# Kernel optimization log

Measured on AMD Instinct MI355X. Metric: run time of the kernel, lower is better.

Reference implementation:

```python
import jax, jax.numpy as jnp
import numpy as np

B, DIM, DIMH, DIMC = 1024, 32, 1024, 512
SQRT_HALF_PI = float(np.sqrt(np.pi / 2.0))
SQRT2 = float(np.sqrt(2.0))


def _gsp(x):
    """gaussian_softplus activation from ConditionalICNN."""
    return (SQRT_HALF_PI * x * jax.scipy.special.erf(x / SQRT2)
            + jnp.exp(-0.5 * x * x) + SQRT_HALF_PI * x) / (2.0 * SQRT_HALF_PI)


def setup_inputs() -> dict:
    key = jax.random.key(0)
    _i = [0]
    def nrm(shape, s=0.05):
        _i[0] += 1
        return jax.random.normal(jax.random.fold_in(key, _i[0]), shape, dtype=jnp.float32) * s
    inp = {
        "x": nrm((B, DIM), 1.0),
        "c": nrm((B, DIMC), 1.0),
        # w0 init: log(exp(1)-1) as in DeepConvexFlow
        "w0": jnp.full((1,), float(np.log(np.e - 1.0)), dtype=jnp.float32),
        "w1": jnp.zeros((1,), dtype=jnp.float32),
        "Wz0_w": nrm((DIMH, DIM)), "Wz0_b": nrm((DIMH,)),
        "Wc0_w": nrm((DIMH, DIMC)), "Wc0_b": nrm((DIMH,)),
        "an0_b": nrm((DIMH,)), "an0_logs": nrm((DIMH,), 0.01),
        "Wz1_w": nrm((DIMH, DIMH)), "Wz1_b": nrm((DIMH,)),
        "Wx1_w": nrm((DIMH, DIM)), "Wx1_b": nrm((DIMH,)),
        "Wc1_w": nrm((DIMH, DIMC)), "Wc1_b": nrm((DIMH,)),
        "an1_b": nrm((DIMH,)), "an1_logs": nrm((DIMH,), 0.01),
        "Wz2_w": nrm((DIMH, DIMH)), "Wz2_b": nrm((DIMH,)),
        "Wx2_w": nrm((DIMH, DIM)), "Wx2_b": nrm((DIMH,)),
        "Wc2_w": nrm((DIMH, DIMC)), "Wc2_b": nrm((DIMH,)),
        "an2_b": nrm((DIMH,)), "an2_logs": nrm((DIMH,), 0.01),
        "Wzout_w": nrm((1, DIMH)), "Wxout_w": nrm((1, DIM)), "Wcout_w": nrm((1, DIMC)),
    }
    return inp


def reference(x, c, w0, w1,
              Wz0_w, Wz0_b, Wc0_w, Wc0_b, an0_b, an0_logs,
              Wz1_w, Wz1_b, Wx1_w, Wx1_b, Wc1_w, Wc1_b, an1_b, an1_logs,
              Wz2_w, Wz2_b, Wx2_w, Wx2_b, Wc2_w, Wc2_b, an2_b, an2_logs,
              Wzout_w, Wxout_w, Wcout_w):
    """ConditionalDeepConvexFlow.forward_transform with exact logdet.
    Returns (f = grad_x F(x), logdet = logabsdet of per-sample Hessian)."""

    def pot(x1, c1):  # scalar convex potential F for one sample
        h = Wz0_w @ x1 + Wz0_b + Wc0_w @ c1 + Wc0_b
        z = _gsp((h + an0_b) * jnp.exp(an0_logs))  # ActNormNoLogdet + act
        for (Wz_w, Wz_b, Wx_w, Wx_b, Wc_w, Wc_b, an_b, an_logs) in (
                (Wz1_w, Wz1_b, Wx1_w, Wx1_b, Wc1_w, Wc1_b, an1_b, an1_logs),
                (Wz2_w, Wz2_b, Wx2_w, Wx2_b, Wc2_w, Wc2_b, an2_b, an2_logs)):
            # PosLinear: softplus(W) with gain 1/in_features
            h = (jax.nn.softplus(Wz_w) @ z) / DIMH + Wz_b \
                + Wx_w @ x1 + Wx_b + Wc_w @ c1 + Wc_b
            z = _gsp((h + an_b) * jnp.exp(an_logs))
        icnn = (jax.nn.softplus(Wzout_w) @ z)[0] / DIMH \
               + (Wxout_w @ x1)[0] + (Wcout_w @ c1)[0]
        return jax.nn.softplus(w1)[0] * icnn \
               + jax.nn.softplus(w0)[0] * 0.5 * jnp.sum(x1 * x1)

    f = jax.vmap(jax.grad(pot))(x, c)          # [B, DIM]
    H = jax.vmap(jax.hessian(pot))(x, c)       # [B, DIM, DIM]
    logdet = jnp.linalg.slogdet(H)[1]          # [B]
    return f, logdet
```

## Files before the change

### kernel.cpp

```cpp
#include <hip/hip_runtime.h>

constexpr int NB   = 1024;
constexpr int NDIM = 32;
constexpr int NH   = 1024;
constexpr int NC   = 512;
constexpr int NS   = 8;
constexpr int KSF  = 8;

constexpr float INV_SQRT2PI = 0.3989422804014327f;
constexpr float SQRT_HALF   = 0.70710678118654752f;
constexpr float SQRT_HPI    = 1.2533141373155003f;

typedef __attribute__((ext_vector_type(8))) short short8;
typedef __attribute__((ext_vector_type(4))) short short4v;
typedef __attribute__((ext_vector_type(4))) float float4v;

__device__ __forceinline__ float sp_f(float x) {
  return (x > 20.f) ? x : log1pf(expf(x));
}

__device__ __forceinline__ short f2bf(float f) {
  union { float f; unsigned u; } x; x.f = f;
  const unsigned r = x.u + 0x7fffu + ((x.u >> 16) & 1u);
  return (short)(r >> 16);
}

__device__ __forceinline__ float bf2f(short s) {
  union { unsigned u; float f; } c;
  c.u = ((unsigned)(unsigned short)s) << 16;
  return c.f;
}

__device__ __forceinline__ void async_ld16(const void* g, void* l) {
  __builtin_amdgcn_global_load_lds(
      (const __attribute__((address_space(1))) void*)g,
      (__attribute__((address_space(3))) void*)l, 16, 0, 0);
}

__global__ __launch_bounds__(256) void k_prep(
    const float* __restrict__ Wz1, const float* __restrict__ Wz2,
    const float* __restrict__ Wzout, const float* __restrict__ Wz0,
    const float* __restrict__ Wx1, const float* __restrict__ Wx2,
    const float* __restrict__ Wc0, const float* __restrict__ Wc1,
    const float* __restrict__ Wc2, const float* __restrict__ Cc,
    short* __restrict__ S1b, short* __restrict__ S1Tb,
    short* __restrict__ S2b, short* __restrict__ S2Tb,
    short* __restrict__ Wc0b, short* __restrict__ Wc1b, short* __restrict__ Wc2b,
    short* __restrict__ Ccb, short* __restrict__ W0Tb,
    short* __restrict__ Wx1Tb, short* __restrict__ Wx2Tb,
    float* __restrict__ so)
{
  const int idx = blockIdx.x * 256 + threadIdx.x;
  const int i = idx >> 10, p = idx & 1023;
  const float v1 = sp_f(Wz1[idx]);
  const short b1 = f2bf(v1);
  S1b[idx] = b1; S1Tb[p * NH + i] = b1;
  const float v2 = sp_f(Wz2[idx]);
  const short b2 = f2bf(v2);
  S2b[idx] = b2; S2Tb[p * NH + i] = b2;
  if (idx < NH) so[idx] = sp_f(Wzout[idx]);
  if (idx < NH * NC) {
    Wc0b[idx] = f2bf(Wc0[idx]);
    Wc1b[idx] = f2bf(Wc1[idx]);
    Wc2b[idx] = f2bf(Wc2[idx]);
  }
  if (idx < NB * NC) Ccb[idx] = f2bf(Cc[idx]);
  if (idx < NDIM * NH) {
    const int j = idx >> 10, pp = idx & 1023;
    W0Tb[idx]  = f2bf(Wz0[pp * NDIM + j]);
    Wx1Tb[idx] = f2bf(Wx1[pp * NDIM + j]);
    Wx2Tb[idx] = f2bf(Wx2[pp * NDIM + j]);
  }
}

__global__ __launch_bounds__(256) void k_gemmx(
    const float* __restrict__ A,
    const float* __restrict__ B0, const float* __restrict__ B1,
    const float* __restrict__ B2,
    float* __restrict__ C0, float* __restrict__ C1, float* __restrict__ C2,
    int ldc,
    const float* __restrict__ bz0, const float* __restrict__ bc0,
    const float* __restrict__ anb0, const float* __restrict__ anl0,
    short* __restrict__ Z0b, float* __restrict__ G0, float* __restrict__ U0)
{
  const float* Bt = (blockIdx.z == 0) ? B0 : (blockIdx.z == 1) ? B1 : B2;
  float* C        = (blockIdx.z == 0) ? C0 : (blockIdx.z == 1) ? C1 : C2;
  __shared__ float As[16][68];
  __shared__ float Bs[16][68];
  const int tid  = threadIdx.y * 16 + threadIdx.x;
  const int arow = tid >> 2;
  const int acol = (tid & 3) << 2;
  const int m0 = blockIdx.y << 6;
  const int n0 = blockIdx.x << 6;

  float acc[4][4];
#pragma unroll
  for (int i = 0; i < 4; ++i)
#pragma unroll
    for (int j = 0; j < 4; ++j) acc[i][j] = 0.f;

  const int R = m0 + arow;
  for (int k0 = 0; k0 < NDIM; k0 += 16) {
    const float4 av = *reinterpret_cast<const float4*>(&A[(size_t)R * NDIM + k0 + acol]);
    As[acol + 0][arow] = av.x; As[acol + 1][arow] = av.y;
    As[acol + 2][arow] = av.z; As[acol + 3][arow] = av.w;
    const float4 bv = *reinterpret_cast<const float4*>(&Bt[(size_t)(n0 + arow) * NDIM + k0 + acol]);
    Bs[acol + 0][arow] = bv.x; Bs[acol + 1][arow] = bv.y;
    Bs[acol + 2][arow] = bv.z; Bs[acol + 3][arow] = bv.w;
    __syncthreads();
#pragma unroll
    for (int kk = 0; kk < 16; ++kk) {
      const float4 a  = *reinterpret_cast<const float4*>(&As[kk][threadIdx.y << 2]);
      const float4 bb = *reinterpret_cast<const float4*>(&Bs[kk][threadIdx.x << 2]);
      const float am[4] = {a.x, a.y, a.z, a.w};
      const float bn[4] = {bb.x, bb.y, bb.z, bb.w};
#pragma unroll
      for (int i2 = 0; i2 < 4; ++i2)
#pragma unroll
        for (int j2 = 0; j2 < 4; ++j2)
          acc[i2][j2] = fmaf(am[i2], bn[j2], acc[i2][j2]);
    }
    __syncthreads();
  }
#pragma unroll
  for (int i2 = 0; i2 < 4; ++i2) {
    const int row = m0 + (threadIdx.y << 2) + i2;
    const int col = n0 + (threadIdx.x << 2);
    float* cp = &C[(size_t)row * ldc + col];
    const float4 cur = *reinterpret_cast<const float4*>(cp);
    float o[4];
    o[0] = acc[i2][0] + cur.x; o[1] = acc[i2][1] + cur.y;
    o[2] = acc[i2][2] + cur.z; o[3] = acc[i2][3] + cur.w;
    if (blockIdx.z == 0) {
      short4v zb;
      float4 g4, u4;
      float gg[4], uu[4];
#pragma unroll
      for (int e = 0; e < 4; ++e) {
        const int cc = col + e;
        const float bias = bz0[cc] + bc0[cc] + anb0[cc];
        const float el = expf(anl0[cc]);
        const float a = (o[e] + bias) * el;
        const float pdf = expf(-0.5f * a * a);
        const float er = erff(a * SQRT_HALF);
        zb[e] = f2bf((SQRT_HPI * a * er + pdf + SQRT_HPI * a) * INV_SQRT2PI);
        gg[e] = 0.5f * (1.f + er) * el;
        uu[e] = pdf * INV_SQRT2PI * el * el;
      }
      const size_t oi = (size_t)row * NH + col;
      *(short4v*)&Z0b[oi] = zb;
      g4.x = gg[0]; g4.y = gg[1]; g4.z = gg[2]; g4.w = gg[3];
      u4.x = uu[0]; u4.y = uu[1]; u4.z = uu[2]; u4.w = uu[3];
      *(float4*)&G0[oi] = g4;
      *(float4*)&U0[oi] = u4;
    } else {
      float4 ov;
      ov.x = o[0]; ov.y = o[1]; ov.z = o[2]; ov.w = o[3];
      *reinterpret_cast<float4*>(cp) = ov;
    }
  }
}

__global__ __launch_bounds__(256) void k_m128(
    const short* __restrict__ A, const short* __restrict__ Bt,
    float* __restrict__ C, float scale, int K, int ldc)
{
  __shared__ short As[128 * 32];
  __shared__ short Bs[128 * 32];
  const int tid  = threadIdx.x;
  const int wave = tid >> 6, lane = tid & 63;
  const int m0 = blockIdx.x << 7, n0 = blockIdx.y << 7;
  const int wm = (wave >> 1) << 6, wn = (wave & 1) << 6;
  const int qd = lane >> 4, md = lane & 15;
  const int sr = lane >> 2;
  const int sc = (lane & 3) << 3;

  float4v acc[4][4];
#pragma unroll
  for (int i = 0; i < 4; ++i)
#pragma unroll
    for (int j = 0; j < 4; ++j) acc[i][j] = (float4v)(0.f);

  for (int k0 = 0; k0 < K; k0 += 32) {
#pragma unroll
    for (int i = 0; i < 2; ++i) {
      const int ch  = wave * 2 + i;
      const int row = ch * 16 + sr;
      async_ld16(&A [(size_t)(m0 + row) * K + k0 + sc], &As[ch * 512]);
      async_ld16(&Bt[(size_t)(n0 + row) * K + k0 + sc], &Bs[ch * 512]);
    }
    __syncthreads();
    short8 af[4], bfr[4];
#pragma unroll
    for (int t = 0; t < 4; ++t) {
      af[t]  = *(const short8*)&As[(wm + t * 16 + md) * 32 + qd * 8];
      bfr[t] = *(const short8*)&Bs[(wn + t * 16 + md) * 32 + qd * 8];
    }
#pragma unroll
    for (int i = 0; i < 4; ++i)
#pragma unroll
      for (int j = 0; j < 4; ++j)
        acc[i][j] = __builtin_amdgcn_mfma_f32_16x16x32_bf16(bfr[j], af[i], acc[i][j], 0, 0, 0);
    __syncthreads();
  }

#pragma unroll
  for (int i = 0; i < 4; ++i) {
    const int rowg = m0 + wm + i * 16 + md;
#pragma unroll
    for (int j = 0; j < 4; ++j) {
      const int colb = n0 + wn + j * 16 + (qd << 2);
      float4 o;
      o.x = acc[i][j][0] * scale; o.y = acc[i][j][1] * scale;
      o.z = acc[i][j][2] * scale; o.w = acc[i][j][3] * scale;
      *reinterpret_cast<float4*>(&C[(size_t)rowg * ldc + colb]) = o;
    }
  }
}

template<int EPI>
__global__ __launch_bounds__(256) void k_mgemm(
    const short* __restrict__ A, const short* __restrict__ Bt,
    short* __restrict__ o1, short* __restrict__ o2,
    const float* __restrict__ gvec, const float* __restrict__ dvec,
    const short* __restrict__ wepiT,
    float scale, int K, int b0)
{
  __shared__ short As[128 * 32];
  const int tid  = threadIdx.x;
  const int wave = tid >> 6, lane = tid & 63;
  const int m0 = blockIdx.x << 7, n0 = blockIdx.y << 6;
  const int wm = (wave >> 1) << 6, wn = (wave & 1) << 5;
  const int qd = lane >> 4, md = lane & 15;
  const int sr = lane >> 2;
  const int sc = (lane & 3) << 3;

  float4v acc[4][2];
#pragma unroll
  for (int i = 0; i < 4; ++i)
#pragma unroll
    for (int j = 0; j < 2; ++j) acc[i][j] = (float4v)(0.f);

  for (int k0 = 0; k0 < K; k0 += 32) {
#pragma unroll
    for (int i = 0; i < 2; ++i) {
      const int ch = wave * 2 + i;
      async_ld16(&A[(size_t)(m0 + ch * 16 + sr) * K + k0 + sc], &As[ch * 512]);
    }
    short8 bfr[2];
#pragma unroll
    for (int t = 0; t < 2; ++t)
      bfr[t] = *(const short8*)&Bt[(size_t)(n0 + wn + t * 16 + md) * K + k0 + qd * 8];
    __syncthreads();
    short8 af[4];
#pragma unroll
    for (int t = 0; t < 4; ++t)
      af[t] = *(const short8*)&As[(wm + t * 16 + md) * 32 + qd * 8];
#pragma unroll
    for (int i = 0; i < 4; ++i)
#pragma unroll
      for (int j = 0; j < 2; ++j)
        acc[i][j] = __builtin_amdgcn_mfma_f32_16x16x32_bf16(bfr[j], af[i], acc[i][j], 0, 0, 0);
    __syncthreads();
  }

  const int bbase = b0 + ((m0 + wm) >> 5);
  const size_t bNH0 = (size_t)bbase * NH, bNH1 = bNH0 + NH;
  float4 dqA[2], dqB[2], ggA[2], ggB[2];
#pragma unroll
  for (int j = 0; j < 2; ++j) {
    const int colb = n0 + wn + j * 16 + (qd << 2);
    dqA[j] = *(const float4*)&dvec[bNH0 + colb];
    dqB[j] = *(const float4*)&dvec[bNH1 + colb];
    if constexpr (EPI == 2) {
      ggA[j] = *(const float4*)&gvec[bNH0 + colb];
      ggB[j] = *(const float4*)&gvec[bNH1 + colb];
    }
  }
#pragma unroll
  for (int i = 0; i < 4; ++i) {
    const int rowg = m0 + wm + i * 16 + md;
    const int j2 = rowg & 31;
#pragma unroll
    for (int j = 0; j < 2; ++j) {
      const int colb = n0 + wn + j * 16 + (qd << 2);
      const short4v wq = *(const short4v*)&wepiT[(size_t)j2 * NH + colb];
      const float4 dq = (i < 2) ? dqA[j] : dqB[j];
      const float dqv[4] = {dq.x, dq.y, dq.z, dq.w};
      float v[4];
      short4v o1v;
#pragma unroll
      for (int r = 0; r < 4; ++r) {
        v[r] = acc[i][j][r] * scale + bf2f(wq[r]);
        o1v[r] = f2bf(v[r] * dqv[r]);
      }
      *(short4v*)&o1[(size_t)rowg * NH + colb] = o1v;
      if constexpr (EPI == 2) {
        const float4 gg = (i < 2) ? ggA[j] : ggB[j];
        const float ggv[4] = {gg.x, gg.y, gg.z, gg.w};
        short4v o2v;
#pragma unroll
        for (int r = 0; r < 4; ++r) o2v[r] = f2bf(v[r] * ggv[r]);
        *(short4v*)&o2[(size_t)rowg * NH + colb] = o2v;
      }
    }
  }
}

__global__ __launch_bounds__(256) void k_mgemm64s(
    const short* __restrict__ A, const short* __restrict__ Bt,
    float* __restrict__ Cpart)
{
  __shared__ short As[64 * 32];
  __shared__ short Bs[64 * 32];
  const int tid  = threadIdx.x;
  const int wave = tid >> 6, lane = tid & 63;
  const int m0 = blockIdx.x << 6, n0 = blockIdx.y << 6;
  const int kb = blockIdx.z << 9;
  const int wm = (wave >> 1) << 5, wn = (wave & 1) << 5;
  const int qd = lane >> 4, md = lane & 15;
  const int sr = lane >> 2;
  const int sc = (lane & 3) << 3;

  float4v acc[2][2];
#pragma unroll
  for (int i = 0; i < 2; ++i)
#pragma unroll
    for (int j = 0; j < 2; ++j) acc[i][j] = (float4v)(0.f);

  for (int k0 = kb; k0 < kb + 512; k0 += 32) {
    const int row = wave * 16 + sr;
    async_ld16(&A [(size_t)(m0 + row) * NH + k0 + sc], &As[wave * 512]);
    async_ld16(&Bt[(size_t)(n0 + row) * NH + k0 + sc], &Bs[wave * 512]);
    __syncthreads();
    short8 af[2], bfr[2];
#pragma unroll
    for (int t = 0; t < 2; ++t) {
      af[t]  = *(const short8*)&As[(wm + t * 16 + md) * 32 + qd * 8];
      bfr[t] = *(const short8*)&Bs[(wn + t * 16 + md) * 32 + qd * 8];
    }
#pragma unroll
    for (int i = 0; i < 2; ++i)
#pragma unroll
      for (int j = 0; j < 2; ++j)
        acc[i][j] = __builtin_amdgcn_mfma_f32_16x16x32_bf16(bfr[j], af[i], acc[i][j], 0, 0, 0);
    __syncthreads();
  }

  float* out = Cpart + (size_t)blockIdx.z * NB * NH;
#pragma unroll
  for (int i = 0; i < 2; ++i) {
    const int rowg = m0 + wm + i * 16 + md;
#pragma unroll
    for (int j = 0; j < 2; ++j) {
      const int colb = n0 + wn + j * 16 + (qd << 2);
      float4 o;
      o.x = acc[i][j][0]; o.y = acc[i][j][1];
      o.z = acc[i][j][2]; o.w = acc[i][j][3];
      *reinterpret_cast<float4*>(&out[(size_t)rowg * NH + colb]) = o;
    }
  }
}

template<int FEPI>
__global__ __launch_bounds__(256) void k_mgemm64f(
    const short* __restrict__ A, const short* __restrict__ Bt,
    const float* __restrict__ auxA, const float* __restrict__ auxB,
    short* __restrict__ ob, float* __restrict__ of1,
    float scale)
{
  __shared__ short As[64 * 32];
  __shared__ short Bs[64 * 32];
  const int tid  = threadIdx.x;
  const int wave = tid >> 6, lane = tid & 63;
  const int m0 = blockIdx.x << 6, n0 = blockIdx.y << 6;
  const int wm = (wave >> 1) << 5, wn = (wave & 1) << 5;
  const int qd = lane >> 4, md = lane & 15;
  const int sr = lane >> 2;
  const int sc = (lane & 3) << 3;

  float4v acc[2][2];
#pragma unroll
  for (int i = 0; i < 2; ++i)
#pragma unroll
    for (int j = 0; j < 2; ++j) acc[i][j] = (float4v)(0.f);

  for (int k0 = 0; k0 < NH; k0 += 32) {
    const int row = wave * 16 + sr;
    async_ld16(&A [(size_t)(m0 + row) * NH + k0 + sc], &As[wave * 512]);
    async_ld16(&Bt[(size_t)(n0 + row) * NH + k0 + sc], &Bs[wave * 512]);
    __syncthreads();
    short8 af[2], bfr[2];
#pragma unroll
    for (int t = 0; t < 2; ++t) {
      af[t]  = *(const short8*)&As[(wm + t * 16 + md) * 32 + qd * 8];
      bfr[t] = *(const short8*)&Bs[(wn + t * 16 + md) * 32 + qd * 8];
    }
#pragma unroll
    for (int i = 0; i < 2; ++i)
#pragma unroll
      for (int j = 0; j < 2; ++j)
        acc[i][j] = __builtin_amdgcn_mfma_f32_16x16x32_bf16(bfr[j], af[i], acc[i][j], 0, 0, 0);
    __syncthreads();
  }

#pragma unroll
  for (int i = 0; i < 2; ++i) {
    const int rowg = m0 + wm + i * 16 + md;
#pragma unroll
    for (int j = 0; j < 2; ++j) {
      const int colb = n0 + wn + j * 16 + (qd << 2);
      const size_t oi = (size_t)rowg * NH + colb;
      const float4 g4 = *(const float4*)&auxA[oi];
      const float4 u4 = *(const float4*)&auxB[oi];
      const float gv[4] = {g4.x, g4.y, g4.z, g4.w};
      const float uv[4] = {u4.x, u4.y, u4.z, u4.w};
      short4v eb;
      float sd[4];
#pragma unroll
      for (int r = 0; r < 4; ++r) {
        const float t = acc[i][j][r] * scale;
        eb[r] = f2bf(t * gv[r]);
        if constexpr (FEPI == 3) sd[r] = sqrtf(fmaxf(t * uv[r], 0.f));
        else                     sd[r] = t * uv[r];
      }
      *(short4v*)&ob[oi] = eb;
      float4 s4; s4.x = sd[0]; s4.y = sd[1]; s4.z = sd[2]; s4.w = sd[3];
      *(float4*)&of1[oi] = s4;
    }
  }
}

__global__ __launch_bounds__(256) void k_act(
    const float* __restrict__ HP2, const float* __restrict__ HPC_l,
    const float* __restrict__ bA, const float* __restrict__ bB,
    const float* __restrict__ bC,
    const float* __restrict__ anb, const float* __restrict__ anl,
    short* __restrict__ Zbf, float* __restrict__ G, float* __restrict__ U,
    float scale)
{
  const int idx = blockIdx.x * 256 + threadIdx.x;
  const int i = idx & 1023;
  const float bias = bA[i] + bB[i] + bC[i] + anb[i];
  const float el = expf(anl[i]);
  const float hc = HPC_l[(size_t)(idx >> 10) * (3 * NH) + i];
  const float hp = (HP2[idx] + HP2[(size_t)NB * NH + idx]) * scale;
  const float a = (hp + hc + bias) * el;
  const float pdf = expf(-0.5f * a * a);
  const float er = erff(a * SQRT_HALF);
  Zbf[idx] = f2bf((SQRT_HPI * a * er + pdf + SQRT_HPI * a) * INV_SQRT2PI);
  G[idx] = 0.5f * (1.f + er) * el;
  U[idx] = pdf * INV_SQRT2PI * el * el;
}

__global__ __launch_bounds__(256) void k_act2(
    const float* __restrict__ HP2, const float* __restrict__ HPC_l,
    const float* __restrict__ bA, const float* __restrict__ bB,
    const float* __restrict__ bC,
    const float* __restrict__ anb, const float* __restrict__ anl,
    const float* __restrict__ so,
    float* __restrict__ SD2, short* __restrict__ D2gbf, float scale)
{
  const int idx = blockIdx.x * 256 + threadIdx.x;
  const int i = idx & 1023;
  const float bias = bA[i] + bB[i] + bC[i] + anb[i];
  const float el = expf(anl[i]);
  const float hc = HPC_l[(size_t)(idx >> 10) * (3 * NH) + i];
  const float hp = (HP2[idx] + HP2[(size_t)NB * NH + idx]) * scale;
  const float a = (hp + hc + bias) * el;
  const float pdf = expf(-0.5f * a * a);
  const float er = erff(a * SQRT_HALF);
  const float g = 0.5f * (1.f + er) * el;
  const float u = pdf * INV_SQRT2PI * el * el;
  const float t2 = so[i] * (1.f / NH);
  SD2[idx] = sqrtf(fmaxf(t2 * u, 0.f));
  D2gbf[idx] = f2bf(t2 * g);
}

__global__ __launch_bounds__(256) void k_scale0(
    const float* __restrict__ G0, const short* __restrict__ W0Tb,
    short* __restrict__ Ah1, int b0)
{
  const int idx = blockIdx.x * 256 + threadIdx.x;
  const int p = idx & 1023, r = idx >> 10;
  const int b = b0 + (r >> 5), j = r & 31;
  Ah1[idx] = f2bf(G0[(size_t)b * NH + p] * bf2f(W0Tb[(size_t)j * NH + p]));
}

__global__ __launch_bounds__(256) void k_fgemm(
    const short* __restrict__ A0, const short* __restrict__ A1,
    const short* __restrict__ A2,
    const short* __restrict__ W0T, const short* __restrict__ W1T,
    const short* __restrict__ W2T,
    float* __restrict__ partF)
{
  const int mb = blockIdx.x;
  const int ks = blockIdx.y;
  const int term = blockIdx.z;
  const short* A  = (term == 0) ? A0 : (term == 1) ? A1 : A2;
  const short* WT = (term == 0) ? W0T : (term == 1) ? W1T : W2T;
  const int wave = threadIdx.x >> 6, lane = threadIdx.x & 63;
  const int qd = lane >> 4, md = lane & 15;
  const int m0 = mb * 128 + wave * 32;
  const int kbeg = ks * (NH / KSF);

  float4v acc[2][2];
#pragma unroll
  for (int i = 0; i < 2; ++i)
#pragma unroll
    for (int j = 0; j < 2; ++j) acc[i][j] = (float4v)(0.f);

  for (int k0 = kbeg; k0 < kbeg + NH / KSF; k0 += 32) {
    const int kk = k0 + qd * 8;
    short8 af[2], bfr[2];
    af[0]  = *(const short8*)&A[(size_t)(m0 + md) * NH + kk];
    af[1]  = *(const short8*)&A[(size_t)(m0 + 16 + md) * NH + kk];
    bfr[0] = *(const short8*)&WT[(size_t)md * NH + kk];
    bfr[1] = *(const short8*)&WT[(size_t)(16 + md) * NH + kk];
#pragma unroll
    for (int i = 0; i < 2; ++i)
#pragma unroll
      for (int j = 0; j < 2; ++j)
        acc[i][j] = __builtin_amdgcn_mfma_f32_16x16x32_bf16(af[i], bfr[j], acc[i][j], 0, 0, 0);
  }

  float* out = &partF[(size_t)(term * KSF + ks) * NB * 32];
#pragma unroll
  for (int i = 0; i < 2; ++i)
#pragma unroll
    for (int j = 0; j < 2; ++j)
#pragma unroll
      for (int r = 0; r < 4; ++r) {
        const int row = m0 + i * 16 + qd * 4 + r;
        const int col = j * 16 + md;
        out[(size_t)row * 32 + col] = acc[i][j][r];
      }
}

__global__ __launch_bounds__(256) void k_fred(
    const float* __restrict__ partF, const float* __restrict__ X,
    const float* __restrict__ Wxout,
    const float* __restrict__ w0p, const float* __restrict__ w1p,
    float* __restrict__ outF)
{
  const int e = blockIdx.x * 256 + threadIdx.x;
  float s = 0.f;
#pragma unroll
  for (int p = 0; p < 3 * KSF; ++p) s += partF[(size_t)p * NB * 32 + e];
  const float spw0 = sp_f(w0p[0]);
  const float spw1 = sp_f(w1p[0]);
  outF[e] = spw1 * (s + Wxout[e & 31]) + spw0 * X[e];
}

__global__ __launch_bounds__(256) void k_gram(
    const short* __restrict__ Q1, const short* __restrict__ Q2,
    const short* __restrict__ W0T, const float* __restrict__ D0,
    float* __restrict__ partH, int b0)
{
  const int ns = blockIdx.x, bl = blockIdx.y;
  const int b = b0 + bl;
  const int wave = threadIdx.x >> 6, lane = threadIdx.x & 63;
  const int wm = (wave >> 1) << 4, wn = (wave & 1) << 4;
  const int qd = lane >> 4, md = lane & 15;
  const int kbeg = ns << 7;
  const size_t rb = (size_t)bl * 32 * NH;

  float4v acc = (float4v)(0.f);

  for (int k0 = kbeg; k0 < kbeg + 128; k0 += 32) {
    const int kk = k0 + qd * 8;
    const short8 ar = *(const short8*)&W0T[(size_t)(wm + md) * NH + kk];
    float dd[8];
    *(float4*)&dd[0] = *(const float4*)&D0[(size_t)b * NH + kk];
    *(float4*)&dd[4] = *(const float4*)&D0[(size_t)b * NH + kk + 4];
    short8 af;
#pragma unroll
    for (int e = 0; e < 8; ++e) af[e] = f2bf(bf2f(ar[e]) * dd[e]);
    const short8 bfr = *(const short8*)&W0T[(size_t)(wn + md) * NH + kk];
    acc = __builtin_amdgcn_mfma_f32_16x16x32_bf16(af, bfr, acc, 0, 0, 0);
  }
#pragma unroll
  for (int l = 0; l < 2; ++l) {
    const short* Q = (l == 0) ? Q1 : Q2;
    for (int k0 = kbeg; k0 < kbeg + 128; k0 += 32) {
      const int kk = k0 + qd * 8;
      const short8 af  = *(const short8*)&Q[rb + (size_t)(wm + md) * NH + kk];
      const short8 bfr = *(const short8*)&Q[rb + (size_t)(wn + md) * NH + kk];
      acc = __builtin_amdgcn_mfma_f32_16x16x32_bf16(af, bfr, acc, 0, 0, 0);
    }
  }

  float* out = &partH[((size_t)bl * NS + ns) * 1024];
#pragma unroll
  for (int r = 0; r < 4; ++r)
    out[(wm + qd * 4 + r) * 32 + (wn + md)] = acc[r];
}

__global__ __launch_bounds__(256) void k_gram2(
    const float* __restrict__ partH,
    const float* __restrict__ w0p, const float* __restrict__ w1p,
    float* __restrict__ outLD, int b0)
{
  const int bl = blockIdx.x, b = b0 + bl, tid = threadIdx.x;
  __shared__ float sH[32][33];
  __shared__ float sred[32];
  const float spw0 = sp_f(w0p[0]);
  const float spw1 = sp_f(w1p[0]);
  const float* base = &partH[(size_t)bl * NS * 1024];
#pragma unroll
  for (int r = 0; r < 4; ++r) {
    const int e = r * 256 + tid;
    float s = 0.f;
#pragma unroll
    for (int ns = 0; ns < NS; ++ns) s += base[ns * 1024 + e];
    float h = s * spw1;
    const int row = e >> 5, col = e & 31;
    if (row == col) h += spw0;
    sH[row][col] = h;
  }
  __syncthreads();

  float ldacc = 0.f;
  for (int c = 0; c < 32; ++c) {
    if (tid >= c && tid < 32) {
      float s = sH[tid][c];
      for (int m = 0; m < c; ++m) s -= sH[tid][m] * sH[c][m];
      sred[tid] = s;
    }
    __syncthreads();
    const float sc = sred[c];
    if (tid >= c && tid < 32) {
      const float lcc = sqrtf(sc);
      sH[tid][c] = (tid == c) ? lcc : sred[tid] / lcc;
    }
    ldacc += logf(sc);
    __syncthreads();
  }
  if (tid == 0) outLD[b] = ldacc;
}

extern "C" void kernel_launch(void* const* d_in, const int* in_sizes, int n_in,
                              void* d_out, int out_size, void* d_ws, size_t ws_size,
                              hipStream_t stream)
{
  const float* X    = (const float*)d_in[0];
  const float* Cc   = (const float*)d_in[1];
  const float* w0   = (const float*)d_in[2];
  const float* w1   = (const float*)d_in[3];
  const float* Wz0w = (const float*)d_in[4];
  const float* Wz0b = (const float*)d_in[5];
  const float* Wc0w = (const float*)d_in[6];
  const float* Wc0b = (const float*)d_in[7];
  const float* an0b = (const float*)d_in[8];
  const float* an0l = (const float*)d_in[9];
  const float* Wz1w = (const float*)d_in[10];
  const float* Wz1b = (const float*)d_in[11];
  const float* Wx1w = (const float*)d_in[12];
  const float* Wx1b = (const float*)d_in[13];
  const float* Wc1w = (const float*)d_in[14];
  const float* Wc1b = (const float*)d_in[15];
  const float* an1b = (const float*)d_in[16];
  const float* an1l = (const float*)d_in[17];
  const float* Wz2w = (const float*)d_in[18];
  const float* Wz2b = (const float*)d_in[19];
  const float* Wx2w = (const float*)d_in[20];
  const float* Wx2b = (const float*)d_in[21];
  const float* Wc2w = (const float*)d_in[22];
  const float* Wc2b = (const float*)d_in[23];
  const float* an2b = (const float*)d_in[24];
  const float* an2l = (const float*)d_in[25];
  const float* Wzoutw = (const float*)d_in[26];
  const float* Wxoutw = (const float*)d_in[27];

  float* ws = (float*)d_ws;
  size_t off = 0;
  auto alloc = [&](size_t n) {
    float* p = ws + off; off += (n + 3) & ~(size_t)3; return p;
  };
  const size_t HH = (size_t)NH * NH;
  const size_t BH = (size_t)NB * NH;

  short* S1b  = (short*)alloc(HH / 2);
  short* S2b  = (short*)alloc(HH / 2);
  short* S1Tb = (short*)alloc(HH / 2);
  short* S2Tb = (short*)alloc(HH / 2);
  short* Wc0bb = (short*)alloc((size_t)NH * NC / 2);
  short* Wc1bb = (short*)alloc((size_t)NH * NC / 2);
  short* Wc2bb = (short*)alloc((size_t)NH * NC / 2);
  short* Ccb  = (short*)alloc((size_t)NB * NC / 2);
  short* W0Tb = (short*)alloc((size_t)NDIM * NH / 2);
  short* Wx1Tb = (short*)alloc((size_t)NDIM * NH / 2);
  short* Wx2Tb = (short*)alloc((size_t)NDIM * NH / 2);
  float* so   = alloc(NH);
  float* HP2  = alloc(2 * BH);
  float* HPC  = alloc((size_t)NB * 3 * NH);
  short* Z0b  = (short*)alloc(BH / 2);
  short* Z1b  = (short*)alloc(BH / 2);
  float* G0   = alloc(BH);
  float* U0   = alloc(BH);
  float* G1   = alloc(BH);
  float* U1   = alloc(BH);
  float* SD2  = alloc(BH);
  short* D2gb = (short*)alloc(BH / 2);
  short* E1b  = (short*)alloc(BH / 2);
  float* SD1  = alloc(BH);
  float* D0   = alloc(BH);
  short* GT0b = (short*)alloc(BH / 2);
  float* partF = alloc((size_t)3 * KSF * NB * 32);

  const size_t avail_f = ws_size / sizeof(float);
  int CB = 32;
  const int cands[6] = {1024, 512, 256, 128, 64, 32};
  for (int ci = 0; ci < 6; ++ci) {
    const size_t need = off + 3 * ((size_t)cands[ci] * 32 * NH / 2 + 4)
                      + (size_t)cands[ci] * NS * 1024 + 64;
    if (need <= avail_f) { CB = cands[ci]; break; }
  }
  const size_t chunk_sh = (size_t)CB * 32 * NH;
  short* Ah1 = (short*)alloc(chunk_sh / 2);
  short* A2b = (short*)alloc(chunk_sh / 2);
  short* Q1b = (short*)alloc(chunk_sh / 2);
  short* Q2b = Ah1;
  float* partH = alloc((size_t)CB * NS * 1024);

  float* outF  = (float*)d_out;
  float* outLD = (float*)d_out + NB * NDIM;

  const dim3 blk2(16, 16);
  const dim3 gridXz(16, NB / 64, 3);
  const dim3 gridE(NB * NH / 256);
  const dim3 grid64s(NB / 64, NH / 64, 2);
  const dim3 grid64u(NB / 64, NH / 64);
  const dim3 gridC(NB / 128, 3 * NH / 128);
  const float invH = 1.0f / (float)NH;

  k_prep<<<dim3(HH / 256), dim3(256), 0, stream>>>(
      Wz1w, Wz2w, Wzoutw, Wz0w, Wx1w, Wx2w, Wc0w, Wc1w, Wc2w, Cc,
      S1b, S1Tb, S2b, S2Tb, Wc0bb, Wc1bb, Wc2bb, Ccb, W0Tb, Wx1Tb, Wx2Tb, so);

  k_m128<<<gridC, dim3(256), 0, stream>>>(Ccb, Wc0bb, HPC, 1.f, NC, 3 * NH);
  k_gemmx<<<gridXz, blk2, 0, stream>>>(X, Wz0w, Wx1w, Wx2w,
                                       HPC + 0 * NH, HPC + 1 * NH, HPC + 2 * NH, 3 * NH,
                                       Wz0b, Wc0b, an0b, an0l, Z0b, G0, U0);

  k_mgemm64s<<<grid64s, dim3(256), 0, stream>>>(Z0b, S1b, HP2);
  k_act<<<gridE, dim3(256), 0, stream>>>(HP2, HPC + 1 * NH, Wz1b, Wx1b, Wc1b,
                                         an1b, an1l, Z1b, G1, U1, invH);
  k_mgemm64s<<<grid64s, dim3(256), 0, stream>>>(Z1b, S2b, HP2);
  k_act2<<<gridE, dim3(256), 0, stream>>>(HP2, HPC + 2 * NH, Wz2b, Wx2b, Wc2b,
                                          an2b, an2l, so, SD2, D2gb, invH);
  k_mgemm64f<3><<<grid64u, dim3(256), 0, stream>>>(D2gb, S2Tb, G1, U1, E1b, SD1, invH);
  k_mgemm64f<4><<<grid64u, dim3(256), 0, stream>>>(E1b, S1Tb, G0, U0, GT0b, D0, invH);

  k_fgemm<<<dim3(8, KSF, 3), dim3(256), 0, stream>>>(
      GT0b, E1b, D2gb, W0Tb, Wx1Tb, Wx2Tb, partF);
  k_fred<<<dim3(NB * 32 / 256), dim3(256), 0, stream>>>(
      partF, X, Wxoutw, w0, w1, outF);

  const dim3 gridJ(CB * 32 / 128, NH / 64);
  const dim3 gridS((size_t)CB * 32 * NH / 256);
  const dim3 gridG(NS, CB);
  for (int b0 = 0; b0 < NB; b0 += CB) {
    k_scale0<<<gridS, dim3(256), 0, stream>>>(G0, W0Tb, Ah1, b0);
    k_mgemm<2><<<gridJ, dim3(256), 0, stream>>>(Ah1, S1b, Q1b, A2b,
                                                G1, SD1, Wx1Tb, invH, NH, b0);
    k_mgemm<1><<<gridJ, dim3(256), 0, stream>>>(A2b, S2b, Q2b, nullptr,
                                                nullptr, SD2, Wx2Tb, invH, NH, b0);
    k_gram<<<gridG, dim3(256), 0, stream>>>(Q1b, Q2b, W0Tb, D0, partH, b0);
    k_gram2<<<dim3(CB), dim3(256), 0, stream>>>(partH, w0, w1, outLD, b0);
  }
}
```

Baseline: 791.9 us.

## Stage B tile in LDS, double K-step, and XOR-swizzle shared layout in k_mgemm

The mgemm main loop now takes K in steps of 64 instead of 32. The Bt operand is staged through shared memory with async loads instead of being read directly from global memory by each wave. Both the A and B shared tiles use an XOR swizzle on 16-byte chunks to avoid LDS bank conflicts when reading MFMA fragments. The intent is to halve the number of barriers per K and coalesce the B loads. The cost is more LDS per block, which may lower occupancy, and the change assumes K is a multiple of 64.

```diff
diff --git a/kernel.cpp b/kernel.cpp
--- a/kernel.cpp
+++ b/kernel.cpp
@@ -226,14 +226,16 @@
     const short* __restrict__ wepiT,
     float scale, int K, int b0)
 {
-  __shared__ short As[128 * 32];
+  __shared__ short As[128 * 64];
+  __shared__ short Bs[64 * 64];
   const int tid  = threadIdx.x;
   const int wave = tid >> 6, lane = tid & 63;
   const int m0 = blockIdx.x << 7, n0 = blockIdx.y << 6;
   const int wm = (wave >> 1) << 6, wn = (wave & 1) << 5;
   const int qd = lane >> 4, md = lane & 15;
-  const int sr = lane >> 2;
-  const int sc = (lane & 3) << 3;
+  const int lr8 = lane >> 3;
+  const int lg  = (lane & 7) ^ lr8;
+  const int mS  = md & 7;
 
   float4v acc[4][2];
 #pragma unroll
@@ -241,26 +243,40 @@
 #pragma unroll
     for (int j = 0; j < 2; ++j) acc[i][j] = (float4v)(0.f);
 
-  for (int k0 = 0; k0 < K; k0 += 32) {
+  for (int k0 = 0; k0 < K; k0 += 64) {
+#pragma unroll
+    for (int i = 0; i < 4; ++i) {
+      const int g8  = wave * 4 + i;
+      const int row = g8 * 8 + lr8;
+      async_ld16(&A[(size_t)(m0 + row) * K + k0 + lg * 8], &As[g8 * 512]);
+    }
 #pragma unroll
     for (int i = 0; i < 2; ++i) {
-      const int ch = wave * 2 + i;
-      async_ld16(&A[(size_t)(m0 + ch * 16 + sr) * K + k0 + sc], &As[ch * 512]);
-    }
-    short8 bfr[2];
-#pragma unroll
-    for (int t = 0; t < 2; ++t)
-      bfr[t] = *(const short8*)&Bt[(size_t)(n0 + wn + t * 16 + md) * K + k0 + qd * 8];
-    __syncthreads();
-    short8 af[4];
-#pragma unroll
-    for (int t = 0; t < 4; ++t)
-      af[t] = *(const short8*)&As[(wm + t * 16 + md) * 32 + qd * 8];
-#pragma unroll
-    for (int i = 0; i < 4; ++i)
-#pragma unroll
-      for (int j = 0; j < 2; ++j)
-        acc[i][j] = __builtin_amdgcn_mfma_f32_16x16x32_bf16(bfr[j], af[i], acc[i][j], 0, 0, 0);
+      const int g8  = wave * 2 + i;
+      const int row = g8 * 8 + lr8;
+      async_ld16(&Bt[(size_t)(n0 + row) * K + k0 + lg * 8], &Bs[g8 * 512]);
+    }
+    __syncthreads();
+#pragma unroll
+    for (int h = 0; h < 2; ++h) {
+      const int cs = h * 4 + qd;
+      short8 af[4], bfr[2];
+#pragma unroll
+      for (int t = 0; t < 4; ++t) {
+        const int r = wm + t * 16 + md;
+        af[t] = *(const short8*)&As[r * 64 + ((cs ^ mS) << 3)];
+      }
+#pragma unroll
+      for (int t = 0; t < 2; ++t) {
+        const int r = wn + t * 16 + md;
+        bfr[t] = *(const short8*)&Bs[r * 64 + ((cs ^ mS) << 3)];
+      }
+#pragma unroll
+      for (int i = 0; i < 4; ++i)
+#pragma unroll
+        for (int j = 0; j < 2; ++j)
+          acc[i][j] = __builtin_amdgcn_mfma_f32_16x16x32_bf16(bfr[j], af[i], acc[i][j], 0, 0, 0);
+    }
     __syncthreads();
   }
 
```

Result: faster. 648.2 us (-18.2%).
